# Kernel optimization log

Measured on AMD Instinct MI355X. Metric: run time of the kernel, lower is better.

## Reference

```python
import jax, jax.numpy as jnp
import numpy as np

EMB = 1024
HEADS = 16
HEAD_DIM = EMB // HEADS


def setup_inputs() -> dict:
    key = jax.random.key(0)
    ks = jax.random.split(key, 6)
    B, S = 4, 1024
    inputs = jax.random.normal(ks[0], (B, S, EMB), dtype=jnp.float32)
    # causal mask: 1.0 where attention is disallowed (added * -1e9 in the layer)
    mask = (1.0 - jnp.tril(jnp.ones((S, S), dtype=jnp.float32)))[None, None, :, :]
    scale = 1.0 / np.sqrt(EMB)
    wq = jax.random.normal(ks[1], (EMB, EMB), dtype=jnp.float32) * scale
    wk = jax.random.normal(ks[2], (EMB, EMB), dtype=jnp.float32) * scale
    wv = jax.random.normal(ks[3], (EMB, EMB), dtype=jnp.float32) * scale
    wo = jax.random.normal(ks[4], (EMB, EMB), dtype=jnp.float32) * scale
    zb = jnp.zeros((EMB,), dtype=jnp.float32)
    return {"inputs": inputs, "mask": mask, "wq": wq, "bq": zb, "wk": wk,
            "bk": zb, "wv": wv, "bv": zb, "wo": wo, "bo": zb}


def _split_heads(t, B):
    # [B, S, E] -> [B, H, S, Dh]
    return t.reshape(B, -1, HEADS, HEAD_DIM).transpose(0, 2, 1, 3)


def reference(inputs, mask, wq, bq, wk, bk, wv, bv, wo, bo):
    B = inputs.shape[0]
    q = _split_heads(inputs @ wq + bq, B)
    k = _split_heads(inputs @ wk + bk, B)
    v = _split_heads(inputs @ wv + bv, B)
    # NOTE: source divides by sqrt(sqrt(head_num)) = head_num**0.25
    scores = jnp.einsum('bhsd,bhtd->bhst', q, k) / jnp.asarray(HEADS, inputs.dtype) ** 0.25
    if mask is not None:
        scores = scores + mask * -1e9
    attn = jax.nn.softmax(scores, axis=-1)
    z = jnp.einsum('bhst,bhtd->bhsd', attn, v)
    # Faithful to source: reshape [B,H,S,Dh] -> [B,S,E] WITHOUT transposing heads back
    z = z.reshape(B, -1, EMB)
    return z @ wo + bo
```

## Files before the change

kernel.cpp:

```cpp
#include <hip/hip_runtime.h>
#include <hip/hip_bf16.h>
#include <stdint.h>

typedef __attribute__((ext_vector_type(8))) short short8;
typedef __attribute__((ext_vector_type(4))) float float4v;

#define SEQ   1024
#define NQKV  3072

__device__ __forceinline__ float bf2f(ushort h) {
    union { uint u; float f; } c; c.u = ((uint)h) << 16; return c.f;
}
__device__ __forceinline__ ushort f2bf(float f) {
    union { uint u; float f; } c; c.f = f;
    uint u = c.u;
    return (ushort)((u + 0x7fffu + ((u >> 16) & 1u)) >> 16);
}
__device__ __forceinline__ uint cvt_pk_bf16(float lo, float hi) {
    uint r;
    asm volatile("v_cvt_pk_bf16_f32 %0, %1, %2" : "=v"(r) : "v"(lo), "v"(hi));
    return r;
}
__device__ __forceinline__ void gl2lds16(const ushort* g, ushort* l) {
    __builtin_amdgcn_global_load_lds(
        (const __attribute__((address_space(1))) unsigned int*)(g),
        (__attribute__((address_space(3))) unsigned int*)(l),
        16, 0, 0);
}

__global__ __launch_bounds__(256) void prep_k(const void* __restrict__ X,
                                              const void* __restrict__ w0,
                                              const void* __restrict__ w1,
                                              const void* __restrict__ w2,
                                              const void* __restrict__ w3,
                                              const void* __restrict__ bq,
                                              const void* __restrict__ bk,
                                              const void* __restrict__ bv,
                                              const void* __restrict__ bo,
                                              ushort* __restrict__ xc,
                                              ushort* __restrict__ biasout,
                                              ushort* __restrict__ wtall,
                                              int* __restrict__ flag) {
    __shared__ int tot;
    __shared__ ushort tile[64][72];
    int t = threadIdx.x;
    if (t == 0) tot = 0;
    __syncthreads();
    uint wv = ((const uint*)X)[t];
    uint e = (wv >> 7) & 0xFFu;
    bool isbf = (e >= 100u && e <= 130u);
    unsigned long long m = __ballot(isbf);
    if ((t & 63) == 0) atomicAdd(&tot, __popcll(m));
    __syncthreads();
    bool isf = (tot <= 128);

    int bi = blockIdx.x;
    if (bi == 0 && t == 0) flag[0] = isf ? 1 : 0;

    if (bi < 4096) {
        if (!isf) return;
        int i = (bi * 256 + t) * 4;
        float4 v = *(const float4*)((const float*)X + i);
        ushort4 o;
        o.x = f2bf(v.x); o.y = f2bf(v.y); o.z = f2bf(v.z); o.w = f2bf(v.w);
        *(ushort4*)(xc + i) = o;
    } else if (bi < 4112) {
        int i = (bi - 4096) * 256 + t;
        int sel = i >> 10, j = i & 1023;
        const void* p = (sel == 0) ? bq : (sel == 1) ? bk : (sel == 2) ? bv : bo;
        biasout[i] = isf ? f2bf(((const float*)p)[j]) : ((const ushort*)p)[j];
    } else {
        int idx = bi - 4112;
        int z = idx >> 8, rem = idx & 255;
        const void* in = (z == 0) ? w0 : (z == 1) ? w1 : (z == 2) ? w2 : w3;
        ushort* out = wtall + (size_t)z * 1024 * 1024;
        int k0 = (rem & 15) * 64, n0 = (rem >> 4) * 64;
        int r = t >> 3, c = (t & 7) * 8;
#pragma unroll
        for (int p = 0; p < 2; p++) {
            int rr = r + p * 32;
            if (isf) {
                const float* src = (const float*)in + (size_t)(k0 + rr) * 1024 + n0 + c;
                float4 v0 = *(const float4*)src;
                float4 v1 = *(const float4*)(src + 4);
                tile[rr][c + 0] = f2bf(v0.x); tile[rr][c + 1] = f2bf(v0.y);
                tile[rr][c + 2] = f2bf(v0.z); tile[rr][c + 3] = f2bf(v0.w);
                tile[rr][c + 4] = f2bf(v1.x); tile[rr][c + 5] = f2bf(v1.y);
                tile[rr][c + 6] = f2bf(v1.z); tile[rr][c + 7] = f2bf(v1.w);
            } else {
                uint4 v = *(const uint4*)((const ushort*)in + (size_t)(k0 + rr) * 1024 + n0 + c);
                *(uint4*)&tile[rr][c] = v;
            }
        }
        __syncthreads();
#pragma unroll
        for (int p = 0; p < 2; p++) {
            int n = r + p * 32;
            ushort vals[8];
#pragma unroll
            for (int j = 0; j < 8; j++) vals[j] = tile[c + j][n];
            *(uint4*)(out + (size_t)(n0 + n) * 1024 + k0 + c) = *(uint4*)vals;
        }
    }
}

__global__ __launch_bounds__(256) void vtrans_k(const ushort* __restrict__ qkv,
                                                ushort* __restrict__ vt) {
    __shared__ ushort tile[64][72];
    int t0 = blockIdx.x * 64;
    int bh = blockIdx.y;
    int b = bh >> 4, h = bh & 15;
    int t = threadIdx.x;
    int r = t >> 3, c = (t & 7) * 8;
#pragma unroll
    for (int p = 0; p < 2; p++) {
        int rr = r + p * 32;
        uint4 v = *(const uint4*)(qkv + (size_t)(b * 1024 + t0 + rr) * NQKV + 2048 + h * 64 + c);
        *(uint4*)&tile[rr][c] = v;
    }
    __syncthreads();
#pragma unroll
    for (int p = 0; p < 2; p++) {
        int d = r + p * 32;
        ushort vals[8];
#pragma unroll
        for (int j = 0; j < 8; j++) vals[j] = tile[c + j][d];
        *(uint4*)(vt + ((size_t)bh * 64 + d) * 1024 + t0 + c) = *(uint4*)vals;
    }
}

template <int BM, bool DUAL>
__global__ __launch_bounds__(256) void gemm_k(const ushort* __restrict__ Araw,
                                              const ushort* __restrict__ Aconv,
                                              const ushort* __restrict__ BT,
                                              const ushort* __restrict__ bias,
                                              void* __restrict__ C,
                                              const int* __restrict__ flag,
                                              int M, int N, int K) {
    constexpr int RM = BM / 32;
    constexpr int AJ = BM / 64;
    __shared__ ushort As[2][BM * 32];
    __shared__ ushort Bs[2][128 * 32];
    int n0 = blockIdx.x * 128, m0 = blockIdx.y * BM;
    int t = threadIdx.x;
    int w = t >> 6, lane = t & 63, q = lane >> 4, ln = lane & 15;
    int wr = w >> 1, wc = w & 1;
    const ushort* A = (*flag) ? Aconv : Araw;

    float4v acc[RM][4];
#pragma unroll
    for (int r = 0; r < RM; r++)
#pragma unroll
        for (int cc = 0; cc < 4; cc++) acc[r][cc] = (float4v){0.f, 0.f, 0.f, 0.f};

#pragma unroll
    for (int j = 0; j < AJ; j++) {
        int c = j * 256 + t;
        int row = c >> 2, s = c & 3;
        int kc = s ^ ((row >> 1) & 3);
        gl2lds16(A + (size_t)(m0 + row) * K + kc * 8, &As[0][c * 8]);
    }
#pragma unroll
    for (int j = 0; j < 2; j++) {
        int c = j * 256 + t;
        int row = c >> 2, s = c & 3;
        int kc = s ^ ((row >> 1) & 3);
        gl2lds16(BT + (size_t)(n0 + row) * K + kc * 8, &Bs[0][c * 8]);
    }

    int nIter = K >> 5;
    for (int kt = 0; kt < nIter; kt++) {
        int cur = kt & 1;
        __syncthreads();
        if (kt + 1 < nIter) {
            int nk0 = (kt + 1) << 5, nxt = cur ^ 1;
#pragma unroll
            for (int j = 0; j < AJ; j++) {
                int c = j * 256 + t;
                int row = c >> 2, s = c & 3;
                int kc = s ^ ((row >> 1) & 3);
                gl2lds16(A + (size_t)(m0 + row) * K + nk0 + kc * 8, &As[nxt][c * 8]);
            }
#pragma unroll
            for (int j = 0; j < 2; j++) {
                int c = j * 256 + t;
                int row = c >> 2, s = c & 3;
                int kc = s ^ ((row >> 1) & 3);
                gl2lds16(BT + (size_t)(n0 + row) * K + nk0 + kc * 8, &Bs[nxt][c * 8]);
            }
        }
        short8 af[RM], bf[4];
#pragma unroll
        for (int r = 0; r < RM; r++) {
            int row = wr * (BM / 2) + r * 16 + ln;
            af[r] = *(const short8*)&As[cur][((row << 2) | (q ^ ((row >> 1) & 3))) * 8];
        }
#pragma unroll
        for (int cc = 0; cc < 4; cc++) {
            int col = wc * 64 + cc * 16 + ln;
            bf[cc] = *(const short8*)&Bs[cur][((col << 2) | (q ^ ((col >> 1) & 3))) * 8];
        }
#pragma unroll
        for (int r = 0; r < RM; r++)
#pragma unroll
            for (int cc = 0; cc < 4; cc++)
                acc[r][cc] = __builtin_amdgcn_mfma_f32_16x16x32_bf16(af[r], bf[cc], acc[r][cc], 0, 0, 0);
    }

    bool outf = DUAL && (*flag != 0);
#pragma unroll
    for (int cc = 0; cc < 4; cc++) {
        int n = n0 + wc * 64 + cc * 16 + ln;
        float bs = bf2f(bias[n]);
#pragma unroll
        for (int r = 0; r < RM; r++) {
#pragma unroll
            for (int i = 0; i < 4; i++) {
                int m = m0 + wr * (BM / 2) + r * 16 + q * 4 + i;
                float v = acc[r][cc][i] + bs;
                if (outf) ((float*)C)[(size_t)m * N + n] = v;
                else      ((ushort*)C)[(size_t)m * N + n] = f2bf(v);
            }
        }
    }
}

__global__ __launch_bounds__(512) void attn_k(const ushort* __restrict__ qkv,
                                              const ushort* __restrict__ vt,
                                              ushort* __restrict__ zp) {
    __shared__ ushort Ks[2][64 * 64];
    __shared__ ushort Vs[2][64 * 64];
    __shared__ ushort P[8][16 * 76];
    int pr = blockIdx.x;
    int bh = blockIdx.y;
    int b = bh >> 4, h = bh & 15;
    int t = threadIdx.x;
    int w = t >> 6;
    int grp = w >> 2;
    int lane = t & 63, q = lane >> 4, ln = lane & 15;

    const float CE = 0.72134752f;

    const ushort* Qp = qkv + (size_t)(b * SEQ) * NQKV + h * 64;
    const ushort* Kp = qkv + (size_t)(b * SEQ) * NQKV + 1024 + h * 64;
    const ushort* Vt = vt + (size_t)bh * 64 * 1024;

    int row0 = t >> 3, kc0 = (t & 7) ^ (row0 & 7);

    int tiB = 15 - pr;
    int ti = grp ? tiB : pr;
    int sw = ti * 64 + (w & 3) * 16;

    short8 aq0 = *(const short8*)(Qp + (size_t)(sw + ln) * NQKV + q * 8);
    short8 aq1 = *(const short8*)(Qp + (size_t)(sw + ln) * NQKV + 32 + q * 8);

    float lp = 0.f;
    float4v o[4];
#pragma unroll
    for (int nb = 0; nb < 4; nb++) o[nb] = (float4v){0.f, 0.f, 0.f, 0.f};

    gl2lds16(Kp + (size_t)row0 * NQKV + kc0 * 8, &Ks[0][t * 8]);
    gl2lds16(Vt + (size_t)row0 * 1024 + kc0 * 8, &Vs[0][t * 8]);

    int srow_l = sw + ln;

    for (int kt = 0; kt <= tiB; kt++) {
        int cur = kt & 1;
        int t0 = kt * 64;
        __syncthreads();
        if (kt < tiB) {
            int nt0 = t0 + 64, nxt = cur ^ 1;
            gl2lds16(Kp + (size_t)(nt0 + row0) * NQKV + kc0 * 8, &Ks[nxt][t * 8]);
            gl2lds16(Vt + (size_t)row0 * 1024 + nt0 + kc0 * 8, &Vs[nxt][t * 8]);
        }
        if (kt <= ti) {
            float4v s[4];
#pragma unroll
            for (int nb = 0; nb < 4; nb++) {
                int row = nb * 16 + ln;
                short8 kf0 = *(const short8*)&Ks[cur][((row << 3) | (q ^ (row & 7))) * 8];
                short8 kf1 = *(const short8*)&Ks[cur][((row << 3) | ((4 + q) ^ (row & 7))) * 8];
                s[nb] = (float4v){0.f, 0.f, 0.f, 0.f};
                s[nb] = __builtin_amdgcn_mfma_f32_16x16x32_bf16(kf0, aq0, s[nb], 0, 0, 0);
                s[nb] = __builtin_amdgcn_mfma_f32_16x16x32_bf16(kf1, aq1, s[nb], 0, 0, 0);
            }
            float p[4][4];
            if (kt < ti) {
#pragma unroll
                for (int nb = 0; nb < 4; nb++)
#pragma unroll
                    for (int i = 0; i < 4; i++) p[nb][i] = exp2f(s[nb][i] * CE);
            } else {
#pragma unroll
                for (int nb = 0; nb < 4; nb++)
#pragma unroll
                    for (int i = 0; i < 4; i++) {
                        int tcol = t0 + nb * 16 + q * 4 + i;
                        p[nb][i] = exp2f((tcol <= srow_l) ? s[nb][i] * CE : -1e30f);
                    }
            }
#pragma unroll
            for (int nb = 0; nb < 4; nb++)
                lp += (p[nb][0] + p[nb][1]) + (p[nb][2] + p[nb][3]);
#pragma unroll
            for (int nb = 0; nb < 4; nb++) {
                uint2 pk;
                pk.x = cvt_pk_bf16(p[nb][0], p[nb][1]);
                pk.y = cvt_pk_bf16(p[nb][2], p[nb][3]);
                *(uint2*)&P[w][ln * 76 + nb * 16 + q * 4] = pk;
            }
            asm volatile("s_waitcnt lgkmcnt(0)\n" ::: "memory");
            short8 ap0 = *(const short8*)&P[w][ln * 76 + q * 8];
            short8 ap1 = *(const short8*)&P[w][ln * 76 + 32 + q * 8];
#pragma unroll
            for (int nb = 0; nb < 4; nb++) {
                int row = nb * 16 + ln;
                short8 bv0 = *(const short8*)&Vs[cur][((row << 3) | (q ^ (row & 7))) * 8];
                short8 bv1 = *(const short8*)&Vs[cur][((row << 3) | ((4 + q) ^ (row & 7))) * 8];
                o[nb] = __builtin_amdgcn_mfma_f32_16x16x32_bf16(ap0, bv0, o[nb], 0, 0, 0);
                o[nb] = __builtin_amdgcn_mfma_f32_16x16x32_bf16(ap1, bv1, o[nb], 0, 0, 0);
            }
        }
    }

    float lred = lp;
    lred += __shfl_xor(lred, 16, 64);
    lred += __shfl_xor(lred, 32, 64);
    float l_i[4];
#pragma unroll
    for (int i = 0; i < 4; i++)
        l_i[i] = __shfl(lred, (q << 4) | (q * 4 + i), 64);

#pragma unroll
    for (int nb = 0; nb < 4; nb++) {
#pragma unroll
        for (int i = 0; i < 4; i++) {
            int srow = sw + q * 4 + i;
            int d = nb * 16 + ln;
            float z = o[nb][i] / l_i[i];
            int sp = h * 64 + (srow >> 4);
            int ep = ((srow & 15) << 6) + d;
            zp[((size_t)(b * SEQ + sp)) * 1024 + ep] = f2bf(z);
        }
    }
}

extern "C" void kernel_launch(void* const* d_in, const int* in_sizes, int n_in,
                              void* d_out, int out_size, void* d_ws, size_t ws_size,
                              hipStream_t stream) {
    const void* X  = d_in[0];
    const void* wq = d_in[2];
    const void* bq = d_in[3];
    const void* wk = d_in[4];
    const void* bk = d_in[5];
    const void* wv = d_in[6];
    const void* bv = d_in[7];
    const void* wo = d_in[8];
    const void* bo = d_in[9];

    char* ws = (char*)d_ws;
    int*    flag  = (int*)ws;
    ushort* biasq = (ushort*)(ws + 4096);
    ushort* WTall = (ushort*)(ws + 12288);
    ushort* Xc    = (ushort*)(ws + 8400896);
    ushort* QKV   = (ushort*)(ws + 16789504);
    ushort* VT    = (ushort*)(ws + 41955328);
    ushort* WTo   = WTall + 3 * 1024 * 1024;
    ushort* ZP    = Xc;

    prep_k<<<5136, 256, 0, stream>>>(X, wq, wk, wv, wo, bq, bk, bv, bo,
                                     Xc, biasq, WTall, flag);
    gemm_k<128, false><<<dim3(24, 32), 256, 0, stream>>>(
        (const ushort*)X, Xc, WTall, biasq, QKV, flag, 4096, NQKV, 1024);
    vtrans_k<<<dim3(16, 64), 256, 0, stream>>>(QKV, VT);
    attn_k<<<dim3(8, 64), 512, 0, stream>>>(QKV, VT, ZP);
    gemm_k<64, true><<<dim3(8, 64), 256, 0, stream>>>(
        ZP, ZP, WTo, biasq + 3072, d_out, flag, 4096, 1024, 1024);
}
```

Before: 187.7 us.

## Fuse V transpose into QKV GEMM epilogue, rebalance causal tiles, add MFMA priority

Drops the separate V-transpose kernel: the QKV GEMM epilogue now also writes the V columns straight into the transposed head-major layout with 4-element vector stores. The attention kernel's pairing of query tiles changes from (pr, 15-pr) to adjacent tiles (2pr, 2pr+1), which shares K/V streaming between the two groups, though per-block work becomes unbalanced across blocks. It also raises wave priority around the MFMA sections with s_setprio. The point is to save a launch and a V round trip through memory and to improve overlap, at the cost of scattered strided stores in the GEMM epilogue.

```diff
diff --git a/kernel.cpp b/kernel.cpp
--- a/kernel.cpp
+++ b/kernel.cpp
@@ -104,37 +104,13 @@
     }
 }
 
-__global__ __launch_bounds__(256) void vtrans_k(const ushort* __restrict__ qkv,
-                                                ushort* __restrict__ vt) {
-    __shared__ ushort tile[64][72];
-    int t0 = blockIdx.x * 64;
-    int bh = blockIdx.y;
-    int b = bh >> 4, h = bh & 15;
-    int t = threadIdx.x;
-    int r = t >> 3, c = (t & 7) * 8;
-#pragma unroll
-    for (int p = 0; p < 2; p++) {
-        int rr = r + p * 32;
-        uint4 v = *(const uint4*)(qkv + (size_t)(b * 1024 + t0 + rr) * NQKV + 2048 + h * 64 + c);
-        *(uint4*)&tile[rr][c] = v;
-    }
-    __syncthreads();
-#pragma unroll
-    for (int p = 0; p < 2; p++) {
-        int d = r + p * 32;
-        ushort vals[8];
-#pragma unroll
-        for (int j = 0; j < 8; j++) vals[j] = tile[c + j][d];
-        *(uint4*)(vt + ((size_t)bh * 64 + d) * 1024 + t0 + c) = *(uint4*)vals;
-    }
-}
-
-template <int BM, bool DUAL>
+template <int BM, bool DUAL, bool WRV>
 __global__ __launch_bounds__(256) void gemm_k(const ushort* __restrict__ Araw,
                                               const ushort* __restrict__ Aconv,
                                               const ushort* __restrict__ BT,
                                               const ushort* __restrict__ bias,
                                               void* __restrict__ C,
+                                              ushort* __restrict__ vt,
                                               const int* __restrict__ flag,
                                               int M, int N, int K) {
     constexpr int RM = BM / 32;
@@ -208,18 +184,27 @@
     }
 
     bool outf = DUAL && (*flag != 0);
+    bool wrv = WRV && (n0 >= 2048);
 #pragma unroll
     for (int cc = 0; cc < 4; cc++) {
         int n = n0 + wc * 64 + cc * 16 + ln;
         float bs = bf2f(bias[n]);
 #pragma unroll
         for (int r = 0; r < RM; r++) {
+            ushort pk[4];
 #pragma unroll
             for (int i = 0; i < 4; i++) {
                 int m = m0 + wr * (BM / 2) + r * 16 + q * 4 + i;
                 float v = acc[r][cc][i] + bs;
                 if (outf) ((float*)C)[(size_t)m * N + n] = v;
                 else      ((ushort*)C)[(size_t)m * N + n] = f2bf(v);
+                pk[i] = f2bf(v);
+            }
+            if (wrv) {
+                int mb = m0 + wr * (BM / 2) + r * 16 + q * 4;
+                int b = mb >> 10, trow = mb & 1023;
+                int h = (n - 2048) >> 6, d = n & 63;
+                *(ushort4*)(vt + (((size_t)(b * 16 + h) * 64 + d) * 1024 + trow)) = *(ushort4*)pk;
             }
         }
     }
@@ -247,8 +232,8 @@
 
     int row0 = t >> 3, kc0 = (t & 7) ^ (row0 & 7);
 
-    int tiB = 15 - pr;
-    int ti = grp ? tiB : pr;
+    int tiB = 2 * pr + 1;
+    int ti = grp ? tiB : (tiB - 1);
     int sw = ti * 64 + (w & 3) * 16;
 
     short8 aq0 = *(const short8*)(Qp + (size_t)(sw + ln) * NQKV + q * 8);
@@ -275,6 +260,7 @@
         }
         if (kt <= ti) {
             float4v s[4];
+            __builtin_amdgcn_s_setprio(1);
 #pragma unroll
             for (int nb = 0; nb < 4; nb++) {
                 int row = nb * 16 + ln;
@@ -284,6 +270,7 @@
                 s[nb] = __builtin_amdgcn_mfma_f32_16x16x32_bf16(kf0, aq0, s[nb], 0, 0, 0);
                 s[nb] = __builtin_amdgcn_mfma_f32_16x16x32_bf16(kf1, aq1, s[nb], 0, 0, 0);
             }
+            __builtin_amdgcn_s_setprio(0);
             float p[4][4];
             if (kt < ti) {
 #pragma unroll
@@ -312,6 +299,7 @@
             asm volatile("s_waitcnt lgkmcnt(0)\n" ::: "memory");
             short8 ap0 = *(const short8*)&P[w][ln * 76 + q * 8];
             short8 ap1 = *(const short8*)&P[w][ln * 76 + 32 + q * 8];
+            __builtin_amdgcn_s_setprio(1);
 #pragma unroll
             for (int nb = 0; nb < 4; nb++) {
                 int row = nb * 16 + ln;
@@ -320,6 +308,7 @@
                 o[nb] = __builtin_amdgcn_mfma_f32_16x16x32_bf16(ap0, bv0, o[nb], 0, 0, 0);
                 o[nb] = __builtin_amdgcn_mfma_f32_16x16x32_bf16(ap1, bv1, o[nb], 0, 0, 0);
             }
+            __builtin_amdgcn_s_setprio(0);
         }
     }
 
@@ -370,10 +359,9 @@
 
     prep_k<<<5136, 256, 0, stream>>>(X, wq, wk, wv, wo, bq, bk, bv, bo,
                                      Xc, biasq, WTall, flag);
-    gemm_k<128, false><<<dim3(24, 32), 256, 0, stream>>>(
-        (const ushort*)X, Xc, WTall, biasq, QKV, flag, 4096, NQKV, 1024);
-    vtrans_k<<<dim3(16, 64), 256, 0, stream>>>(QKV, VT);
+    gemm_k<128, false, true><<<dim3(24, 32), 256, 0, stream>>>(
+        (const ushort*)X, Xc, WTall, biasq, QKV, VT, flag, 4096, NQKV, 1024);
     attn_k<<<dim3(8, 64), 512, 0, stream>>>(QKV, VT, ZP);
-    gemm_k<64, true><<<dim3(8, 64), 256, 0, stream>>>(
-        ZP, ZP, WTo, biasq + 3072, d_out, flag, 4096, 1024, 1024);
-}
+    gemm_k<64, true, false><<<dim3(8, 64), 256, 0, stream>>>(
+        ZP, ZP, WTo, biasq + 3072, d_out, nullptr, flag, 4096, 1024, 1024);
+}
```

New measurement: 195.3 us. 1.04x slower.
